# Performance work log

Measured on AMD Instinct MI355X. Metric: run time of the kernel, lower is better.

## Reference

```python
import jax, jax.numpy as jnp
import numpy as np

N_NODES = 100000

def setup_inputs() -> dict:
    key = jax.random.key(0)
    k1, k2, k3, k4 = jax.random.split(key, 4)
    nfeat, nhid = 128, 128
    features = jax.random.normal(k1, (N_NODES, nfeat), dtype=jnp.float32)
    edges = jax.random.randint(k2, (2, 1600000), 0, N_NODES, dtype=jnp.int64)
    # Linear(nfeature, nhidden) params (PyTorch layout: W [out, in], b [out])
    bound = 1.0 / np.sqrt(nfeat)
    W = jax.random.uniform(k3, (nhid, nfeat), dtype=jnp.float32, minval=-bound, maxval=bound)
    b = jax.random.uniform(k4, (nhid,), dtype=jnp.float32, minval=-bound, maxval=bound)
    return {"features": features, "edges": edges, "W": W, "b": b}

def reference(features, edges, W, b):
    n = features.shape[0]
    # add self loops
    loops = jnp.arange(n, dtype=edges.dtype)
    row = jnp.concatenate([edges[0], loops])  # source
    col = jnp.concatenate([edges[1], loops])  # target
    # linear transform
    x = features @ W.T + b  # [N, nhid]
    # degree over source indices (PyG message uses degree(row, size[0]))
    deg = jax.ops.segment_sum(jnp.ones_like(row, dtype=x.dtype), row, num_segments=n)
    dis = jax.lax.rsqrt(deg)  # deg >= 1 thanks to self loops
    norm = dis[row] * dis[col]  # [E']
    msgs = norm[:, None] * x[row]  # gather + scale, [E', nhid]
    out = jax.ops.segment_sum(msgs, col, num_segments=n)  # scatter-add to targets
    return out
```

## Files before the change

kernel.cpp:

```cpp
#include <hip/hip_runtime.h>

#define NFEAT 128
#define CH 25600
#define CH2 (CH / 2)

typedef __attribute__((ext_vector_type(8))) short bf16x8;
typedef __attribute__((ext_vector_type(4))) float f32x4;

static __device__ __forceinline__ short f2bf(float f) {
    unsigned u = __builtin_bit_cast(unsigned, f);
    unsigned r = (u + 0x7fff + ((u >> 16) & 1)) >> 16;
    return (short)r;
}
static __device__ __forceinline__ float bflo(unsigned u) {
    return __builtin_bit_cast(float, u << 16);
}
static __device__ __forceinline__ float bfhi(unsigned u) {
    return __builtin_bit_cast(float, u & 0xffff0000u);
}

__launch_bounds__(256)
__global__ void hist16_kernel(const int* __restrict__ rows, const int* __restrict__ cols,
                              unsigned int* __restrict__ ph_row, unsigned int* __restrict__ ph_col,
                              int* __restrict__ rank, int E, int n, int W, int log_epb) {
    __shared__ unsigned int h[CH2];
    const int b = blockIdx.x;
    const int c0 = blockIdx.y * CH;
    const int z = blockIdx.z;
    const int* __restrict__ keys = z ? cols : rows;
    unsigned int* __restrict__ ph = z ? ph_col : ph_row;

    for (int i = threadIdx.x; i < CH2; i += 256) h[i] = 0;
    __syncthreads();

    const int lo = b << log_epb;
    const int hi = min(E, lo + (1 << log_epb));
    const int t = threadIdx.x;

    int full = (hi - lo) >> 10;
    for (int it = 0; it < full; ++it) {
        int e0 = lo + (it << 10) + t * 4;
        int4 kk = *(const int4*)(keys + e0);
        int k0 = kk.x - c0, k1 = kk.y - c0, k2 = kk.z - c0, k3 = kk.w - c0;
        if ((unsigned)k0 < CH) {
            unsigned old = atomicAdd(&h[k0 >> 1], 1u << ((k0 & 1) * 16));
            if (z) rank[e0 + 0] = (old >> ((k0 & 1) * 16)) & 0xffff;
        }
        if ((unsigned)k1 < CH) {
            unsigned old = atomicAdd(&h[k1 >> 1], 1u << ((k1 & 1) * 16));
            if (z) rank[e0 + 1] = (old >> ((k1 & 1) * 16)) & 0xffff;
        }
        if ((unsigned)k2 < CH) {
            unsigned old = atomicAdd(&h[k2 >> 1], 1u << ((k2 & 1) * 16));
            if (z) rank[e0 + 2] = (old >> ((k2 & 1) * 16)) & 0xffff;
        }
        if ((unsigned)k3 < CH) {
            unsigned old = atomicAdd(&h[k3 >> 1], 1u << ((k3 & 1) * 16));
            if (z) rank[e0 + 3] = (old >> ((k3 & 1) * 16)) & 0xffff;
        }
    }
    for (int e = lo + (full << 10) + t; e < hi; e += 256) {
        int k = keys[e] - c0;
        if ((unsigned)k < CH) {
            unsigned old = atomicAdd(&h[k >> 1], 1u << ((k & 1) * 16));
            if (z) rank[e] = (old >> ((k & 1) * 16)) & 0xffff;
        }
    }
    __syncthreads();

    int wbase = c0 >> 1;
    for (int i = threadIdx.x; i < CH2; i += 256) {
        int w = wbase + i;
        if (w < W) ph[(size_t)b * W + w] = h[i];
    }
}

__global__ void cum_kernel(const unsigned short* __restrict__ ph_row,
                           unsigned short* __restrict__ ph_col,
                           float* __restrict__ dis, int* __restrict__ colcnt, int NB, int n) {
    int k = blockIdx.x * 256 + threadIdx.x;
    if (k >= n) return;
    int rs = 0;
    for (int b = 0; b < NB; ++b) rs += ph_row[(size_t)b * n + k];
    dis[k] = rsqrtf(1.0f + (float)rs);
    int acc = 0;
    for (int b = 0; b < NB; ++b) {
        int v = ph_col[(size_t)b * n + k];
        ph_col[(size_t)b * n + k] = (unsigned short)acc;
        acc += v;
    }
    colcnt[k] = acc;
}

__global__ void scan_bsum_kernel(const int* __restrict__ cnt, int* __restrict__ bsum, int n) {
    __shared__ int s[256];
    int base = blockIdx.x * 1024;
    int t = threadIdx.x;
    int v = 0;
#pragma unroll
    for (int i = 0; i < 4; ++i) {
        int idx = base + t * 4 + i;
        if (idx < n) v += cnt[idx];
    }
    s[t] = v;
    __syncthreads();
    for (int o = 128; o > 0; o >>= 1) {
        if (t < o) s[t] += s[t + o];
        __syncthreads();
    }
    if (t == 0) bsum[blockIdx.x] = s[0];
}

__global__ void scan_top_kernel(int* __restrict__ bsum, int nb) {
    __shared__ int s[256];
    int t = threadIdx.x;
    int v = (t < nb) ? bsum[t] : 0;
    s[t] = v;
    __syncthreads();
    for (int o = 1; o < 256; o <<= 1) {
        int add = (t >= o) ? s[t - o] : 0;
        __syncthreads();
        s[t] += add;
        __syncthreads();
    }
    if (t < nb) bsum[t] = s[t] - v;
}

__global__ void scan_write_kernel(const int* __restrict__ cnt, const int* __restrict__ bsum,
                                  int* __restrict__ off, int n) {
    __shared__ int s[256];
    int base = blockIdx.x * 1024;
    int t = threadIdx.x;
    int v[4];
    int sum = 0;
#pragma unroll
    for (int i = 0; i < 4; ++i) {
        int idx = base + t * 4 + i;
        v[i] = (idx < n) ? cnt[idx] : 0;
        sum += v[i];
    }
    s[t] = sum;
    __syncthreads();
    for (int o = 1; o < 256; o <<= 1) {
        int add = (t >= o) ? s[t - o] : 0;
        __syncthreads();
        s[t] += add;
        __syncthreads();
    }
    int p = bsum[blockIdx.x] + s[t] - sum;
#pragma unroll
    for (int i = 0; i < 4; ++i) {
        int idx = base + t * 4 + i;
        if (idx < n) { off[idx] = p; p += v[i]; }
    }
}

__global__ void scatter2_kernel(const int* __restrict__ rows, const int* __restrict__ cols,
                                const int* __restrict__ rank, const unsigned short* __restrict__ ph_col,
                                const int* __restrict__ off, int* __restrict__ rows_buf,
                                int E, int n, int log_epb) {
    int base = blockIdx.x * 1024 + threadIdx.x;
#pragma unroll
    for (int u = 0; u < 4; ++u) {
        int e = base + u * 256;
        if (e < E) {
            int k = cols[e];
            int b = e >> log_epb;
            int pos = off[k] + (int)ph_col[(size_t)b * n + k] + rank[e];
            rows_buf[pos] = rows[e];
        }
    }
}

__launch_bounds__(256)
__global__ void gemm_bf16_kernel(const float* __restrict__ feat, const float* __restrict__ W,
                                 const float* __restrict__ b, unsigned short* __restrict__ x16, int n) {
    __shared__ short wb[16384];

    const int t = threadIdx.x;

    {
        int c = t >> 1;
        int kbase = (t & 1) * 64;
        int ct = c >> 4;
        int cl = c & 15;
#pragma unroll
        for (int kc = 0; kc < 8; ++kc) {
            int k0 = kbase + kc * 8;
            const float4* src = (const float4*)(W + (size_t)c * NFEAT + k0);
            float4 fa = src[0];
            float4 fb = src[1];
            float fv[8] = {fa.x, fa.y, fa.z, fa.w, fb.x, fb.y, fb.z, fb.w};
            short h8[8];
#pragma unroll
            for (int i = 0; i < 8; ++i) h8[i] = f2bf(fv[i]);
            int kq = k0 >> 5;
            int lane = ((k0 & 31) >> 3) * 16 + cl;
            int idx = ((ct * 4 + kq) * 64 + lane) * 8;
            *(bf16x8*)&wb[idx] = *(bf16x8*)h8;
        }
    }
    __syncthreads();

    const int lane = t & 63;
    const int w = t >> 6;
    const int r0 = blockIdx.x * 64 + w * 16;
    const int arow = r0 + (lane & 15);
    const int koff = (lane >> 4) * 8;

    bf16x8 a[4];
#pragma unroll
    for (int kq = 0; kq < 4; ++kq) {
        float fv[8] = {0, 0, 0, 0, 0, 0, 0, 0};
        if (arow < n) {
            const float4* src = (const float4*)(feat + (size_t)arow * NFEAT + kq * 32 + koff);
            float4 fa = src[0];
            float4 fb = src[1];
            fv[0] = fa.x; fv[1] = fa.y; fv[2] = fa.z; fv[3] = fa.w;
            fv[4] = fb.x; fv[5] = fb.y; fv[6] = fb.z; fv[7] = fb.w;
        }
        short h8[8];
#pragma unroll
        for (int i = 0; i < 8; ++i) h8[i] = f2bf(fv[i]);
        a[kq] = *(bf16x8*)h8;
    }

#pragma unroll
    for (int ct = 0; ct < 8; ++ct) {
        f32x4 acc = {0.f, 0.f, 0.f, 0.f};
#pragma unroll
        for (int kq = 0; kq < 4; ++kq) {
            int idx = ((ct * 4 + kq) * 64 + lane) * 8;
            bf16x8 bh = *(const bf16x8*)&wb[idx];
            acc = __builtin_amdgcn_mfma_f32_16x16x32_bf16(a[kq], bh, acc, 0, 0, 0);
        }
        int col = ct * 16 + (lane & 15);
        float bb = b[col];
#pragma unroll
        for (int reg = 0; reg < 4; ++reg) {
            int row = r0 + (lane >> 4) * 4 + reg;
            if (row < n) x16[(size_t)row * NFEAT + col] = (unsigned short)f2bf(acc[reg] + bb);
        }
    }
}

__launch_bounds__(256)
__global__ void gather_kernel(const int* __restrict__ rows_buf, const int* __restrict__ off,
                              const int* __restrict__ cnt, const unsigned short* __restrict__ x16,
                              const float* __restrict__ dis, float* __restrict__ out, int n) {
    int lane = threadIdx.x & 63;
    int q = lane >> 4;
    int fq = lane & 15;
    int c = blockIdx.x * 4 + (threadIdx.x >> 6);
    if (c >= n) return;

    float disc = dis[c];
    int start = off[c];
    int len = cnt[c];
    const uint4* xv = (const uint4*)x16;

    float a0 = 0.f, a1 = 0.f, a2 = 0.f, a3 = 0.f, a4 = 0.f, a5 = 0.f, a6 = 0.f, a7 = 0.f;

    for (int base = 0; base < len; base += 64) {
        int m = min(64, len - base);
        int r_l = 0;
        float nrm_l = 0.0f;
        if (lane < m) {
            r_l = rows_buf[start + base + lane];
            nrm_l = dis[r_l] * disc;
        }
        int quads = (m + 3) >> 2;
#pragma unroll 4
        for (int jj = 0; jj < quads; ++jj) {
            int src = 4 * jj + q;
            int r = __shfl(r_l, src);
            float nm = __shfl(nrm_l, src);
            if (src < m) {
                uint4 v = xv[(size_t)r * 16 + fq];
                a0 = fmaf(bflo(v.x), nm, a0); a1 = fmaf(bfhi(v.x), nm, a1);
                a2 = fmaf(bflo(v.y), nm, a2); a3 = fmaf(bfhi(v.y), nm, a3);
                a4 = fmaf(bflo(v.z), nm, a4); a5 = fmaf(bfhi(v.z), nm, a5);
                a6 = fmaf(bflo(v.w), nm, a6); a7 = fmaf(bfhi(v.w), nm, a7);
            }
        }
    }

    a0 += __shfl_xor(a0, 16); a1 += __shfl_xor(a1, 16);
    a2 += __shfl_xor(a2, 16); a3 += __shfl_xor(a3, 16);
    a4 += __shfl_xor(a4, 16); a5 += __shfl_xor(a5, 16);
    a6 += __shfl_xor(a6, 16); a7 += __shfl_xor(a7, 16);
    a0 += __shfl_xor(a0, 32); a1 += __shfl_xor(a1, 32);
    a2 += __shfl_xor(a2, 32); a3 += __shfl_xor(a3, 32);
    a4 += __shfl_xor(a4, 32); a5 += __shfl_xor(a5, 32);
    a6 += __shfl_xor(a6, 32); a7 += __shfl_xor(a7, 32);

    if (q == 0) {
        float sl = disc * disc;
        uint4 v = xv[(size_t)c * 16 + fq];
        a0 = fmaf(bflo(v.x), sl, a0); a1 = fmaf(bfhi(v.x), sl, a1);
        a2 = fmaf(bflo(v.y), sl, a2); a3 = fmaf(bfhi(v.y), sl, a3);
        a4 = fmaf(bflo(v.z), sl, a4); a5 = fmaf(bfhi(v.z), sl, a5);
        a6 = fmaf(bflo(v.w), sl, a6); a7 = fmaf(bfhi(v.w), sl, a7);
        float4* o = (float4*)(out + (size_t)c * NFEAT + fq * 8);
        o[0] = make_float4(a0, a1, a2, a3);
        o[1] = make_float4(a4, a5, a6, a7);
    }
}

extern "C" void kernel_launch(void* const* d_in, const int* in_sizes, int n_in,
                              void* d_out, int out_size, void* d_ws, size_t ws_size,
                              hipStream_t stream) {
    const float* feat = (const float*)d_in[0];
    const int*   edges = (const int*)d_in[1];
    const float* W = (const float*)d_in[2];
    const float* b = (const float*)d_in[3];
    float* out = (float*)d_out;

    int n = in_sizes[0] / NFEAT;
    int E = in_sizes[1] / 2;
    const int* row = edges;
    const int* col = edges + E;

    int Wd = (n + 1) / 2;
    int nchunk = (n + CH - 1) / CH;

    size_t fixed = (size_t)n * 64 + 3 * (size_t)n + 2 * (size_t)E + 256;
    int log_epb = 16;
    int NB = (E + (1 << 16) - 1) >> 16;
    for (int lg = 14; lg <= 16; ++lg) {
        int nb_try = (E + (1 << lg) - 1) >> lg;
        size_t words = fixed + 2 * (size_t)nb_try * Wd;
        if (words * 4 <= ws_size) { log_epb = lg; NB = nb_try; break; }
    }

    unsigned short* x16 = (unsigned short*)d_ws;
    float* dis      = (float*)(x16 + (size_t)n * NFEAT);
    int*   colcnt   = (int*)(dis + n);
    int*   off      = colcnt + n;
    int*   rows_buf = off + n;
    int*   rank     = rows_buf + E;
    int*   bsum     = rank + E;
    unsigned int* ph_row = (unsigned int*)(bsum + 256);
    unsigned int* ph_col = ph_row + (size_t)NB * Wd;

    int nb = (n + 1023) / 1024;

    dim3 hgrid(NB, nchunk, 2);
    hist16_kernel<<<hgrid, 256, 0, stream>>>(row, col, ph_row, ph_col, rank, E, n, Wd, log_epb);

    cum_kernel<<<(n + 255) / 256, 256, 0, stream>>>((const unsigned short*)ph_row,
                                                    (unsigned short*)ph_col, dis, colcnt, NB, n);

    scan_bsum_kernel<<<nb, 256, 0, stream>>>(colcnt, bsum, n);
    scan_top_kernel<<<1, 256, 0, stream>>>(bsum, nb);
    scan_write_kernel<<<nb, 256, 0, stream>>>(colcnt, bsum, off, n);

    scatter2_kernel<<<(E + 1023) / 1024, 256, 0, stream>>>(row, col, rank,
                                                           (const unsigned short*)ph_col,
                                                           off, rows_buf, E, n, log_epb);

    gemm_bf16_kernel<<<(n + 63) / 64, 256, 0, stream>>>(feat, W, b, x16, n);

    gather_kernel<<<(n + 3) / 4, 256, 0, stream>>>(rows_buf, off, colcnt, x16, dis, out, n);
}
```

Measured before the change: 335.3 us.

## Split row/col histograms, share one histogram buffer, store ranks as 16-bit

The fused row/col histogram kernel is split into separate row and column passes that run one after another and reuse a single per-block histogram buffer, halving its workspace footprint. Edge ranks are now stored as 16-bit values instead of 32-bit, cutting rank write and read traffic. The smaller workspace lets the edges-per-block selection pick smaller blocks, giving more parallelism, but it adds two extra kernel launches and serializes the row and column histogram work.

```diff
diff --git a/kernel.cpp b/kernel.cpp
--- a/kernel.cpp
+++ b/kernel.cpp
@@ -20,15 +20,49 @@
 }
 
 __launch_bounds__(256)
-__global__ void hist16_kernel(const int* __restrict__ rows, const int* __restrict__ cols,
-                              unsigned int* __restrict__ ph_row, unsigned int* __restrict__ ph_col,
-                              int* __restrict__ rank, int E, int n, int W, int log_epb) {
+__global__ void hist_row_kernel(const int* __restrict__ keys, unsigned int* __restrict__ ph,
+                                int E, int n, int Wd, int log_epb) {
     __shared__ unsigned int h[CH2];
     const int b = blockIdx.x;
     const int c0 = blockIdx.y * CH;
-    const int z = blockIdx.z;
-    const int* __restrict__ keys = z ? cols : rows;
-    unsigned int* __restrict__ ph = z ? ph_col : ph_row;
+
+    for (int i = threadIdx.x; i < CH2; i += 256) h[i] = 0;
+    __syncthreads();
+
+    const int lo = b << log_epb;
+    const int hi = min(E, lo + (1 << log_epb));
+    const int t = threadIdx.x;
+
+    int full = (hi - lo) >> 10;
+    for (int it = 0; it < full; ++it) {
+        int e0 = lo + (it << 10) + t * 4;
+        int4 kk = *(const int4*)(keys + e0);
+        int k0 = kk.x - c0, k1 = kk.y - c0, k2 = kk.z - c0, k3 = kk.w - c0;
+        if ((unsigned)k0 < CH) atomicAdd(&h[k0 >> 1], 1u << ((k0 & 1) * 16));
+        if ((unsigned)k1 < CH) atomicAdd(&h[k1 >> 1], 1u << ((k1 & 1) * 16));
+        if ((unsigned)k2 < CH) atomicAdd(&h[k2 >> 1], 1u << ((k2 & 1) * 16));
+        if ((unsigned)k3 < CH) atomicAdd(&h[k3 >> 1], 1u << ((k3 & 1) * 16));
+    }
+    for (int e = lo + (full << 10) + t; e < hi; e += 256) {
+        int k = keys[e] - c0;
+        if ((unsigned)k < CH) atomicAdd(&h[k >> 1], 1u << ((k & 1) * 16));
+    }
+    __syncthreads();
+
+    int wbase = c0 >> 1;
+    for (int i = threadIdx.x; i < CH2; i += 256) {
+        int w = wbase + i;
+        if (w < Wd) ph[(size_t)b * Wd + w] = h[i];
+    }
+}
+
+__launch_bounds__(256)
+__global__ void hist_col_kernel(const int* __restrict__ keys, unsigned int* __restrict__ ph,
+                                unsigned short* __restrict__ rank16,
+                                int E, int n, int Wd, int log_epb) {
+    __shared__ unsigned int h[CH2];
+    const int b = blockIdx.x;
+    const int c0 = blockIdx.y * CH;
 
     for (int i = threadIdx.x; i < CH2; i += 256) h[i] = 0;
     __syncthreads();
@@ -44,26 +78,26 @@
         int k0 = kk.x - c0, k1 = kk.y - c0, k2 = kk.z - c0, k3 = kk.w - c0;
         if ((unsigned)k0 < CH) {
             unsigned old = atomicAdd(&h[k0 >> 1], 1u << ((k0 & 1) * 16));
-            if (z) rank[e0 + 0] = (old >> ((k0 & 1) * 16)) & 0xffff;
+            rank16[e0 + 0] = (unsigned short)((old >> ((k0 & 1) * 16)) & 0xffff);
         }
         if ((unsigned)k1 < CH) {
             unsigned old = atomicAdd(&h[k1 >> 1], 1u << ((k1 & 1) * 16));
-            if (z) rank[e0 + 1] = (old >> ((k1 & 1) * 16)) & 0xffff;
+            rank16[e0 + 1] = (unsigned short)((old >> ((k1 & 1) * 16)) & 0xffff);
         }
         if ((unsigned)k2 < CH) {
             unsigned old = atomicAdd(&h[k2 >> 1], 1u << ((k2 & 1) * 16));
-            if (z) rank[e0 + 2] = (old >> ((k2 & 1) * 16)) & 0xffff;
+            rank16[e0 + 2] = (unsigned short)((old >> ((k2 & 1) * 16)) & 0xffff);
         }
         if ((unsigned)k3 < CH) {
             unsigned old = atomicAdd(&h[k3 >> 1], 1u << ((k3 & 1) * 16));
-            if (z) rank[e0 + 3] = (old >> ((k3 & 1) * 16)) & 0xffff;
+            rank16[e0 + 3] = (unsigned short)((old >> ((k3 & 1) * 16)) & 0xffff);
         }
     }
     for (int e = lo + (full << 10) + t; e < hi; e += 256) {
         int k = keys[e] - c0;
         if ((unsigned)k < CH) {
             unsigned old = atomicAdd(&h[k >> 1], 1u << ((k & 1) * 16));
-            if (z) rank[e] = (old >> ((k & 1) * 16)) & 0xffff;
+            rank16[e] = (unsigned short)((old >> ((k & 1) * 16)) & 0xffff);
         }
     }
     __syncthreads();
@@ -71,22 +105,27 @@
     int wbase = c0 >> 1;
     for (int i = threadIdx.x; i < CH2; i += 256) {
         int w = wbase + i;
-        if (w < W) ph[(size_t)b * W + w] = h[i];
-    }
-}
-
-__global__ void cum_kernel(const unsigned short* __restrict__ ph_row,
-                           unsigned short* __restrict__ ph_col,
-                           float* __restrict__ dis, int* __restrict__ colcnt, int NB, int n) {
+        if (w < Wd) ph[(size_t)b * Wd + w] = h[i];
+    }
+}
+
+__global__ void cum_row_kernel(const unsigned short* __restrict__ ph16,
+                               float* __restrict__ dis, int NB, int n, int S) {
     int k = blockIdx.x * 256 + threadIdx.x;
     if (k >= n) return;
     int rs = 0;
-    for (int b = 0; b < NB; ++b) rs += ph_row[(size_t)b * n + k];
+    for (int b = 0; b < NB; ++b) rs += ph16[(size_t)b * S + k];
     dis[k] = rsqrtf(1.0f + (float)rs);
+}
+
+__global__ void cum_col_kernel(unsigned short* __restrict__ ph16,
+                               int* __restrict__ colcnt, int NB, int n, int S) {
+    int k = blockIdx.x * 256 + threadIdx.x;
+    if (k >= n) return;
     int acc = 0;
     for (int b = 0; b < NB; ++b) {
-        int v = ph_col[(size_t)b * n + k];
-        ph_col[(size_t)b * n + k] = (unsigned short)acc;
+        int v = ph16[(size_t)b * S + k];
+        ph16[(size_t)b * S + k] = (unsigned short)acc;
         acc += v;
     }
     colcnt[k] = acc;
@@ -156,9 +195,10 @@
 }
 
 __global__ void scatter2_kernel(const int* __restrict__ rows, const int* __restrict__ cols,
-                                const int* __restrict__ rank, const unsigned short* __restrict__ ph_col,
+                                const unsigned short* __restrict__ rank16,
+                                const unsigned short* __restrict__ ph16,
                                 const int* __restrict__ off, int* __restrict__ rows_buf,
-                                int E, int n, int log_epb) {
+                                int E, int n, int S, int log_epb) {
     int base = blockIdx.x * 1024 + threadIdx.x;
 #pragma unroll
     for (int u = 0; u < 4; ++u) {
@@ -166,7 +206,7 @@
         if (e < E) {
             int k = cols[e];
             int b = e >> log_epb;
-            int pos = off[k] + (int)ph_col[(size_t)b * n + k] + rank[e];
+            int pos = off[k] + (int)ph16[(size_t)b * S + k] + (int)rank16[e];
             rows_buf[pos] = rows[e];
         }
     }
@@ -322,14 +362,16 @@
     const int* col = edges + E;
 
     int Wd = (n + 1) / 2;
+    int S = 2 * Wd;
     int nchunk = (n + CH - 1) / CH;
 
-    size_t fixed = (size_t)n * 64 + 3 * (size_t)n + 2 * (size_t)E + 256;
+    size_t fixedW = (size_t)n * 64 + 3 * (size_t)n + (size_t)E + (size_t)(E + 1) / 2 + 256;
+
     int log_epb = 16;
     int NB = (E + (1 << 16) - 1) >> 16;
     for (int lg = 14; lg <= 16; ++lg) {
         int nb_try = (E + (1 << lg) - 1) >> lg;
-        size_t words = fixed + 2 * (size_t)nb_try * Wd;
+        size_t words = fixedW + (size_t)nb_try * Wd;
         if (words * 4 <= ws_size) { log_epb = lg; NB = nb_try; break; }
     }
 
@@ -338,26 +380,26 @@
     int*   colcnt   = (int*)(dis + n);
     int*   off      = colcnt + n;
     int*   rows_buf = off + n;
-    int*   rank     = rows_buf + E;
-    int*   bsum     = rank + E;
-    unsigned int* ph_row = (unsigned int*)(bsum + 256);
-    unsigned int* ph_col = ph_row + (size_t)NB * Wd;
+    unsigned short* rank16 = (unsigned short*)(rows_buf + E);
+    int*   bsum     = (int*)(rank16 + ((size_t)(E + 1) / 2) * 2);
+    unsigned int* ph = (unsigned int*)(bsum + 256);
 
     int nb = (n + 1023) / 1024;
 
-    dim3 hgrid(NB, nchunk, 2);
-    hist16_kernel<<<hgrid, 256, 0, stream>>>(row, col, ph_row, ph_col, rank, E, n, Wd, log_epb);
-
-    cum_kernel<<<(n + 255) / 256, 256, 0, stream>>>((const unsigned short*)ph_row,
-                                                    (unsigned short*)ph_col, dis, colcnt, NB, n);
+    dim3 hgrid(NB, nchunk);
+    hist_row_kernel<<<hgrid, 256, 0, stream>>>(row, ph, E, n, Wd, log_epb);
+    cum_row_kernel<<<(n + 255) / 256, 256, 0, stream>>>((const unsigned short*)ph, dis, NB, n, S);
+
+    hist_col_kernel<<<hgrid, 256, 0, stream>>>(col, ph, rank16, E, n, Wd, log_epb);
+    cum_col_kernel<<<(n + 255) / 256, 256, 0, stream>>>((unsigned short*)ph, colcnt, NB, n, S);
 
     scan_bsum_kernel<<<nb, 256, 0, stream>>>(colcnt, bsum, n);
     scan_top_kernel<<<1, 256, 0, stream>>>(bsum, nb);
     scan_write_kernel<<<nb, 256, 0, stream>>>(colcnt, bsum, off, n);
 
-    scatter2_kernel<<<(E + 1023) / 1024, 256, 0, stream>>>(row, col, rank,
-                                                           (const unsigned short*)ph_col,
-                                                           off, rows_buf, E, n, log_epb);
+    scatter2_kernel<<<(E + 1023) / 1024, 256, 0, stream>>>(row, col, rank16,
+                                                           (const unsigned short*)ph,
+                                                           off, rows_buf, E, n, S, log_epb);
 
     gemm_bf16_kernel<<<(n + 63) / 64, 256, 0, stream>>>(feat, W, b, x16, n);
 
```

Result: no change. 336.2 us (+0.3%).
